# Kernel optimization log

Measured on AMD Instinct MI355X. Metric: run time of the kernel, lower is better.

Reference implementation:

```python
import jax, jax.numpy as jnp
import numpy as np

B, N, D, H, E = 4, 4096, 1024, 16, 256
HD = D // H  # head_dim = 64


def setup_inputs() -> dict:
    key = jax.random.key(0)
    k1, k2, k3, k4, k5 = jax.random.split(key, 5)
    scale = 1.0 / np.sqrt(D)
    return {
        "x": jax.random.normal(k1, (B, N, D), dtype=jnp.float32),
        "proj_weight_all": jax.random.normal(k2, (N, E), dtype=jnp.float32) * (1.0 / np.sqrt(N)),
        "W_q": jax.random.normal(k3, (D, D), dtype=jnp.float32) * scale,
        "W_k": jax.random.normal(k4, (D, D), dtype=jnp.float32) * scale,
        "W_v": jax.random.normal(k5, (D, D), dtype=jnp.float32) * scale,
    }


def reference(x, proj_weight_all, W_q, W_k, W_v):
    # QKV projections: [B,N,D] @ [D,D] -> [B,N,D]
    q = jnp.einsum('bnd,de->bne', x, W_q)
    k = jnp.einsum('bnd,de->bne', x, W_k)
    v = jnp.einsum('bnd,de->bne', x, W_v)
    # split heads -> [B,H,N,hd]
    split = lambda t: t.reshape(B, N, H, HD).transpose(0, 2, 1, 3)
    qh, kh, vh = split(q), split(k), split(v)
    # low-rank sequence projection of K/V: [B,H,N,hd] x [N,E] -> [B,H,E,hd]
    k_proj = jnp.einsum('bhnd,ne->bhed', kh, proj_weight_all)
    v_proj = jnp.einsum('bhnd,ne->bhed', vh, proj_weight_all)
    # attention over projected length E (dropout p=0 -> identity)
    scores = jnp.einsum('bhnd,bhed->bhne', qh, k_proj) / jnp.sqrt(jnp.float32(HD))
    attn = jax.nn.softmax(scores, axis=-1)  # [B,H,N,E]
    out = jnp.einsum('bhne,bhed->bhnd', attn, v_proj)
    # concat heads -> [B,N,D]
    return out.transpose(0, 2, 1, 3).reshape(B, N, D)
```

## Files before the change

### kernel.cpp

```cpp
#include <hip/hip_runtime.h>
#include <hip/hip_bf16.h>

#define B_ 4
#define N_ 4096
#define D_ 1024
#define H_ 16
#define E_ 256
#define HD_ 64

typedef __attribute__((ext_vector_type(8))) short bf16x8;
typedef __attribute__((ext_vector_type(4))) short shortx4;
typedef __attribute__((ext_vector_type(4))) float floatx4;

__device__ inline short f2bf(float f) {
  __hip_bfloat16 h = __float2bfloat16(f);
  short s;
  __builtin_memcpy(&s, &h, 2);
  return s;
}

__device__ inline void gld_lds16(const short* g, short* l) {
  __builtin_amdgcn_global_load_lds(
      (const __attribute__((address_space(1))) void*)g,
      (__attribute__((address_space(3))) void*)l, 16, 0, 0);
}

template <bool CAST_COPY>
__device__ inline void transpose_body(const float* __restrict__ src,
                                      short* __restrict__ dstT,
                                      short* __restrict__ dstC,
                                      int R, int C) {
  __shared__ float tile[32][33];
  int c0 = blockIdx.x * 32;
  int r0 = blockIdx.y * 32;
  int tx = threadIdx.x;
  int ty = threadIdx.y;
#pragma unroll
  for (int i = 0; i < 4; ++i) {
    int r = ty * 4 + i;
    float v = src[(size_t)(r0 + r) * C + (c0 + tx)];
    tile[r][tx] = v;
    if constexpr (CAST_COPY)
      dstC[(size_t)(r0 + r) * C + (c0 + tx)] = f2bf(v);
  }
  __syncthreads();
#pragma unroll
  for (int i = 0; i < 4; ++i) {
    int c = ty * 4 + i;
    dstT[(size_t)(c0 + c) * R + (r0 + tx)] = f2bf(tile[tx][c]);
  }
}

__global__ void transpose_x_kernel(const float* __restrict__ x,
                                   short* __restrict__ xtb,
                                   short* __restrict__ xb) {
  int b = blockIdx.z;
  transpose_body<true>(x + (size_t)b * N_ * D_, xtb + (size_t)b * D_ * N_,
                       xb + (size_t)b * N_ * D_, N_, D_);
}

__global__ void transpose_w_kernel(const float* __restrict__ Wq,
                                   const float* __restrict__ Wk,
                                   const float* __restrict__ Wv,
                                   short* __restrict__ WqT,
                                   short* __restrict__ WkT,
                                   short* __restrict__ WvT) {
  int z = blockIdx.z;
  const float* src = (z == 0) ? Wq : (z == 1) ? Wk : Wv;
  short* dst = (z == 0) ? WqT : (z == 1) ? WkT : WvT;
  transpose_body<false>(src, dst, nullptr, D_, D_);
}

__global__ void transpose_p_kernel(const float* __restrict__ proj,
                                   short* __restrict__ projT) {
  transpose_body<false>(proj, projT, nullptr, N_, E_);
}

__global__ void cast_f32_bf16_kernel(const float* __restrict__ in,
                                     short* __restrict__ out) {
  int i = (blockIdx.x * 256 + threadIdx.x) * 4;
  const float4 v = *(const float4*)(in + i);
  shortx4 o;
  o[0] = f2bf(v.x); o[1] = f2bf(v.y); o[2] = f2bf(v.z); o[3] = f2bf(v.w);
  *(shortx4*)(out + i) = o;
}

__global__ __launch_bounds__(256) void gemm128_bt_kernel(
    const short* __restrict__ Ag, const short* __restrict__ Btg,
    short* __restrict__ Cg, int M, int Nc, int K,
    long sA, long sB, long sC) {
  __shared__ short lds_a[128 * 32];
  __shared__ short lds_b[128 * 32];
  int tid = threadIdx.x;
  int lane = tid & 63;
  int w = tid >> 6;
  int l16 = lane & 15;
  int quad = lane >> 4;
  int wm = w >> 1, wn = w & 1;
  int m0 = blockIdx.x * 128, n0 = blockIdx.y * 128;

  const short* A = Ag + (size_t)blockIdx.z * sA;
  const short* Bt = Btg + (size_t)blockIdx.z * sB;
  short* C = Cg + (size_t)blockIdx.z * sC;

  int srow = tid >> 2;
  int skcol = (tid & 3) * 8;
  const short* ag = A + (size_t)(m0 + srow) * K + skcol;
  const short* bg = Bt + (size_t)(n0 + srow) * K + skcol;
  short* la = lds_a + tid * 8;
  short* lb = lds_b + tid * 8;
  const size_t half = (size_t)64 * K;

  floatx4 acc[4][4];
#pragma unroll
  for (int i = 0; i < 4; ++i)
#pragma unroll
    for (int j = 0; j < 4; ++j) acc[i][j] = (floatx4){0.f, 0.f, 0.f, 0.f};

  for (int k = 0; k < K; k += 32) {
    gld_lds16(ag + k, la);
    gld_lds16(ag + half + k, la + 64 * 32);
    gld_lds16(bg + k, lb);
    gld_lds16(bg + half + k, lb + 64 * 32);
    __syncthreads();

    bf16x8 af[4], bf[4];
#pragma unroll
    for (int mt = 0; mt < 4; ++mt)
      af[mt] = *(const bf16x8*)(lds_a + (wm * 64 + mt * 16 + l16) * 32 + quad * 8);
#pragma unroll
    for (int nt = 0; nt < 4; ++nt)
      bf[nt] = *(const bf16x8*)(lds_b + (wn * 64 + nt * 16 + l16) * 32 + quad * 8);
#pragma unroll
    for (int mt = 0; mt < 4; ++mt)
#pragma unroll
      for (int nt = 0; nt < 4; ++nt)
        acc[mt][nt] = __builtin_amdgcn_mfma_f32_16x16x32_bf16(af[mt], bf[nt], acc[mt][nt], 0, 0, 0);
    __syncthreads();
  }

#pragma unroll
  for (int mt = 0; mt < 4; ++mt)
#pragma unroll
    for (int nt = 0; nt < 4; ++nt)
#pragma unroll
      for (int r = 0; r < 4; ++r) {
        size_t row = (size_t)(m0 + wm * 64 + mt * 16 + quad * 4 + r);
        size_t col = (size_t)(n0 + wn * 64 + nt * 16 + l16);
        C[row * Nc + col] = f2bf(acc[mt][nt][r]);
      }
}

__global__ __launch_bounds__(256) void gemm128_splitk_kernel(
    const short* __restrict__ Ag, const short* __restrict__ Btg,
    float* __restrict__ Cfg, int M, int Nc, int K, int KS,
    long sA, long sB, long sC) {
  __shared__ short lds_a[128 * 32];
  __shared__ short lds_b[128 * 32];
  int tid = threadIdx.x;
  int lane = tid & 63;
  int w = tid >> 6;
  int l16 = lane & 15;
  int quad = lane >> 4;
  int wm = w >> 1, wn = w & 1;
  int m0 = blockIdx.x * 128, n0 = blockIdx.y * 128;
  int bz = blockIdx.z / KS;
  int ks = blockIdx.z % KS;
  int kchunk = K / KS;
  int k0 = ks * kchunk;

  const short* A = Ag + (size_t)bz * sA;
  const short* Bt = Btg + (size_t)bz * sB;
  float* Cf = Cfg + (size_t)bz * sC;

  int srow = tid >> 2;
  int skcol = (tid & 3) * 8;
  const short* ag = A + (size_t)(m0 + srow) * K + skcol;
  const short* bg = Bt + (size_t)(n0 + srow) * K + skcol;
  short* la = lds_a + tid * 8;
  short* lb = lds_b + tid * 8;
  const size_t half = (size_t)64 * K;

  floatx4 acc[4][4];
#pragma unroll
  for (int i = 0; i < 4; ++i)
#pragma unroll
    for (int j = 0; j < 4; ++j) acc[i][j] = (floatx4){0.f, 0.f, 0.f, 0.f};

  for (int k = k0; k < k0 + kchunk; k += 32) {
    gld_lds16(ag + k, la);
    gld_lds16(ag + half + k, la + 64 * 32);
    gld_lds16(bg + k, lb);
    gld_lds16(bg + half + k, lb + 64 * 32);
    __syncthreads();

    bf16x8 af[4], bf[4];
#pragma unroll
    for (int mt = 0; mt < 4; ++mt)
      af[mt] = *(const bf16x8*)(lds_a + (wm * 64 + mt * 16 + l16) * 32 + quad * 8);
#pragma unroll
    for (int nt = 0; nt < 4; ++nt)
      bf[nt] = *(const bf16x8*)(lds_b + (wn * 64 + nt * 16 + l16) * 32 + quad * 8);
#pragma unroll
    for (int mt = 0; mt < 4; ++mt)
#pragma unroll
      for (int nt = 0; nt < 4; ++nt)
        acc[mt][nt] = __builtin_amdgcn_mfma_f32_16x16x32_bf16(af[mt], bf[nt], acc[mt][nt], 0, 0, 0);
    __syncthreads();
  }

#pragma unroll
  for (int mt = 0; mt < 4; ++mt)
#pragma unroll
    for (int nt = 0; nt < 4; ++nt)
#pragma unroll
      for (int r = 0; r < 4; ++r) {
        size_t row = (size_t)(m0 + wm * 64 + mt * 16 + quad * 4 + r);
        size_t col = (size_t)(n0 + wn * 64 + nt * 16 + l16);
        atomicAdd(&Cf[row * Nc + col], acc[mt][nt][r]);
      }
}

__global__ __launch_bounds__(256) void gemm_kv_kernel(
    const short* __restrict__ xp, const short* __restrict__ WkT,
    const short* __restrict__ WvT, short* __restrict__ kpb,
    short* __restrict__ vpT) {
  int tid = threadIdx.x;
  int w = tid >> 6;
  int lane = tid & 63;
  int l16 = lane & 15;
  int quad = lane >> 4;
  int m_base = blockIdx.x * 64 + (w >> 1) * 32;
  int n_base = blockIdx.y * 64 + (w & 1) * 32;
  int b = blockIdx.z;

  const short* Ab = xp + (size_t)b * E_ * D_;
  short* Ck = kpb + (size_t)b * E_ * D_;
  short* Cv = vpT + (size_t)b * D_ * E_;

  floatx4 acck[2][2], accv[2][2];
#pragma unroll
  for (int i = 0; i < 2; ++i)
#pragma unroll
    for (int j = 0; j < 2; ++j) {
      acck[i][j] = (floatx4){0.f, 0.f, 0.f, 0.f};
      accv[i][j] = (floatx4){0.f, 0.f, 0.f, 0.f};
    }

  for (int k = 0; k < D_; k += 32) {
    bf16x8 a[2], bk[2], bv[2];
#pragma unroll
    for (int mt = 0; mt < 2; ++mt)
      a[mt] = *(const bf16x8*)(Ab + (size_t)(m_base + mt * 16 + l16) * D_ + k + quad * 8);
#pragma unroll
    for (int nt = 0; nt < 2; ++nt) {
      size_t off = (size_t)(n_base + nt * 16 + l16) * D_ + k + quad * 8;
      bk[nt] = *(const bf16x8*)(WkT + off);
      bv[nt] = *(const bf16x8*)(WvT + off);
    }
#pragma unroll
    for (int mt = 0; mt < 2; ++mt)
#pragma unroll
      for (int nt = 0; nt < 2; ++nt) {
        acck[mt][nt] = __builtin_amdgcn_mfma_f32_16x16x32_bf16(a[mt], bk[nt], acck[mt][nt], 0, 0, 0);
        accv[mt][nt] = __builtin_amdgcn_mfma_f32_16x16x32_bf16(a[mt], bv[nt], accv[mt][nt], 0, 0, 0);
      }
  }

#pragma unroll
  for (int mt = 0; mt < 2; ++mt)
#pragma unroll
    for (int nt = 0; nt < 2; ++nt)
#pragma unroll
      for (int r = 0; r < 4; ++r) {
        size_t row = (size_t)(m_base + mt * 16 + quad * 4 + r);
        size_t col = (size_t)(n_base + nt * 16 + l16);
        Ck[row * D_ + col] = f2bf(acck[mt][nt][r]);
        Cv[col * E_ + row] = f2bf(accv[mt][nt][r]);
      }
}

__global__ __launch_bounds__(512) void attn_kernel(
    const short* __restrict__ q,
    const short* __restrict__ kp,
    const short* __restrict__ vpT,
    float* __restrict__ out) {
  __shared__ short lds_kp_p[17408];
  __shared__ short lds_vp[16384];

  int tid = threadIdx.x;
  int w = tid >> 6;
  int lane = tid & 63;
  int l16 = lane & 15;
  int quad = lane >> 4;
  int n0 = blockIdx.x * 128;
  int h = blockIdx.y;
  int b = blockIdx.z;

  {
    const short* kpg = kp + (size_t)b * E_ * D_ + h * 64;
    int r0 = tid >> 3;
    int sseg = (tid & 7) ^ (r0 & 7);
#pragma unroll
    for (int j = 0; j < 4; ++j)
      gld_lds16(kpg + (size_t)(r0 + j * 64) * D_ + sseg * 8,
                lds_kp_p + j * 4096 + tid * 8);
  }
  {
    const short* vpg = vpT + (size_t)b * D_ * E_ + (size_t)(h * 64) * E_;
    int s1 = tid & 31;
    int rb = tid >> 5;
    int sseg = (s1 & 24) | ((s1 & 7) ^ (rb & 7));
#pragma unroll
    for (int j = 0; j < 4; ++j)
      gld_lds16(vpg + (size_t)(rb + j * 16) * E_ + sseg * 8,
                lds_vp + j * 4096 + tid * 8);
  }

  const short* qbase = q + ((size_t)(b * N_ + n0 + w * 16 + l16)) * D_ + h * 64;
  bf16x8 qf0 = *(const bf16x8*)(qbase + quad * 8);
  bf16x8 qf1 = *(const bf16x8*)(qbase + 32 + quad * 8);

  __syncthreads();

  floatx4 s[16];
#pragma unroll
  for (int t = 0; t < 16; ++t) s[t] = (floatx4){0.f, 0.f, 0.f, 0.f};

  int sw = l16 & 7;
#pragma unroll
  for (int t = 0; t < 16; ++t) {
    int r = t * 16 + l16;
    const short* rowp = lds_kp_p + r * 64;
    bf16x8 a0 = *(const bf16x8*)(rowp + ((quad) ^ sw) * 8);
    bf16x8 a1 = *(const bf16x8*)(rowp + ((4 + quad) ^ sw) * 8);
    s[t] = __builtin_amdgcn_mfma_f32_16x16x32_bf16(a0, qf0, s[t], 0, 0, 0);
    s[t] = __builtin_amdgcn_mfma_f32_16x16x32_bf16(a1, qf1, s[t], 0, 0, 0);
  }

  float mx = -1e30f;
#pragma unroll
  for (int t = 0; t < 16; ++t)
#pragma unroll
    for (int r = 0; r < 4; ++r) {
      s[t][r] *= 0.125f;
      mx = fmaxf(mx, s[t][r]);
    }
  mx = fmaxf(mx, __shfl_xor(mx, 16, 64));
  mx = fmaxf(mx, __shfl_xor(mx, 32, 64));

  float lsum = 0.f;
#pragma unroll
  for (int t = 0; t < 16; ++t)
#pragma unroll
    for (int r = 0; r < 4; ++r) {
      s[t][r] = __expf(s[t][r] - mx);
      lsum += s[t][r];
    }
  lsum += __shfl_xor(lsum, 16, 64);
  lsum += __shfl_xor(lsum, 32, 64);

  __syncthreads();

  short* pbase = lds_kp_p + w * 2176;
  floatx4 o4[4];
#pragma unroll
  for (int t2 = 0; t2 < 4; ++t2) o4[t2] = (floatx4){0.f, 0.f, 0.f, 0.f};

#pragma unroll
  for (int hf = 0; hf < 2; ++hf) {
#pragma unroll
    for (int t = 0; t < 8; ++t)
#pragma unroll
      for (int r = 0; r < 4; ++r)
        pbase[l16 * 136 + t * 16 + quad * 4 + r] = f2bf(s[hf * 8 + t][r]);

#pragma unroll
    for (int es2 = 0; es2 < 4; ++es2) {
      bf16x8 pa = *(const bf16x8*)(pbase + l16 * 136 + es2 * 32 + quad * 8);
      int es = hf * 4 + es2;
#pragma unroll
      for (int t2 = 0; t2 < 4; ++t2) {
        int rr = t2 * 16 + l16;
        int seg = es * 4 + quad;
        int sg = (seg & 24) | ((seg & 7) ^ sw);
        bf16x8 vf = *(const bf16x8*)(lds_vp + rr * 256 + sg * 8);
        o4[t2] = __builtin_amdgcn_mfma_f32_16x16x32_bf16(pa, vf, o4[t2], 0, 0, 0);
      }
    }
  }

  float linv[4];
#pragma unroll
  for (int r = 0; r < 4; ++r)
    linv[r] = 1.0f / __shfl(lsum, (lane & 48) | (quad * 4 + r), 64);

#pragma unroll
  for (int r = 0; r < 4; ++r) {
    int n = n0 + w * 16 + quad * 4 + r;
#pragma unroll
    for (int t2 = 0; t2 < 4; ++t2)
      out[((size_t)(b * N_ + n)) * D_ + h * 64 + t2 * 16 + l16] = o4[t2][r] * linv[r];
  }
}

extern "C" void kernel_launch(void* const* d_in, const int* in_sizes, int n_in,
                              void* d_out, int out_size, void* d_ws, size_t ws_size,
                              hipStream_t stream) {
  const float* x    = (const float*)d_in[0];
  const float* proj = (const float*)d_in[1];
  const float* Wq   = (const float*)d_in[2];
  const float* Wk   = (const float*)d_in[3];
  const float* Wv   = (const float*)d_in[4];
  float* out = (float*)d_out;

  short* p = (short*)d_ws;
  short* xtb_qb = p; p += (size_t)B_ * D_ * N_;
  short* xb     = p; p += (size_t)B_ * N_ * D_;
  short* WqT    = p; p += (size_t)D_ * D_;
  short* WkT    = p; p += (size_t)D_ * D_;
  short* WvT    = p; p += (size_t)D_ * D_;
  short* projT  = p; p += (size_t)E_ * N_;
  short* xp     = p; p += (size_t)B_ * E_ * D_;
  short* kpb    = p; p += (size_t)B_ * E_ * D_;
  short* vpT    = p; p += (size_t)B_ * D_ * E_;
  float* xp_f32 = (float*)p;
  short* xtb = xtb_qb;
  short* qb  = xtb_qb;

  dim3 blkT(32, 8);
  transpose_x_kernel<<<dim3(D_ / 32, N_ / 32, B_), blkT, 0, stream>>>(x, xtb, xb);
  transpose_w_kernel<<<dim3(D_ / 32, D_ / 32, 3), blkT, 0, stream>>>(Wq, Wk, Wv, WqT, WkT, WvT);
  transpose_p_kernel<<<dim3(E_ / 32, N_ / 32, 1), blkT, 0, stream>>>(proj, projT);

  hipMemsetAsync(xp_f32, 0, (size_t)B_ * E_ * D_ * sizeof(float), stream);
  const int KS = 8;
  gemm128_splitk_kernel<<<dim3(E_ / 128, D_ / 128, B_ * KS), 256, 0, stream>>>(
      projT, xtb, xp_f32, E_, D_, N_, KS, 0, (long)D_ * N_, (long)E_ * D_);
  cast_f32_bf16_kernel<<<(B_ * E_ * D_) / 1024, 256, 0, stream>>>(xp_f32, xp);

  gemm128_bt_kernel<<<dim3((B_ * N_) / 128, D_ / 128, 1), 256, 0, stream>>>(
      xb, WqT, qb, B_ * N_, D_, D_, 0, 0, 0);

  gemm_kv_kernel<<<dim3(E_ / 64, D_ / 64, B_), 256, 0, stream>>>(
      xp, WkT, WvT, kpb, vpT);

  attn_kernel<<<dim3(N_ / 128, H_, B_), 512, 0, stream>>>(qb, kpb, vpT, out);
}
```

Measured before the change: 302.2 us.

## Replace Q-projection GEMM with 256x256 tile, pipelined, swizzled-LDS kernel

Replaces the 128x128 single-buffered Q GEMM with a 512-thread 256x256 tile kernel. It double-buffers 128 KB of LDS, XOR-swizzles the LDS layout and interleaves async global-to-LDS loads with MFMA phases using explicit waitcnt, barriers and setprio. It also remaps block IDs for better L2 locality. This aims to hide load latency, cut LDS bank conflicts and raise operand reuse, at the cost of one block per CU and fewer blocks overall (256).

Result: faster. 285.6 us (-5.5%).

```diff
diff --git a/kernel.cpp b/kernel.cpp
--- a/kernel.cpp
+++ b/kernel.cpp
@@ -85,70 +85,171 @@
   *(shortx4*)(out + i) = o;
 }
 
-__global__ __launch_bounds__(256) void gemm128_bt_kernel(
+__device__ inline bf16x8 frag256(const short* slab, int row, int q) {
+  int a = (row << 6) + (q << 4);
+  a ^= ((a >> 7) & 7) << 4;
+  return *(const bf16x8*)(slab + (a >> 1));
+}
+
+#define G_BAR() __builtin_amdgcn_s_barrier()
+#define G_LGK0() asm volatile("s_waitcnt lgkmcnt(0)" ::: "memory")
+#define G_VM6() asm volatile("s_waitcnt vmcnt(6)" ::: "memory")
+#define G_VM0() asm volatile("s_waitcnt vmcnt(0)" ::: "memory")
+#define G_PRIO1() __builtin_amdgcn_s_setprio(1)
+#define G_PRIO0() __builtin_amdgcn_s_setprio(0)
+
+__global__ __launch_bounds__(512) void gemm256_bt_kernel(
     const short* __restrict__ Ag, const short* __restrict__ Btg,
-    short* __restrict__ Cg, int M, int Nc, int K,
-    long sA, long sB, long sC) {
-  __shared__ short lds_a[128 * 32];
-  __shared__ short lds_b[128 * 32];
+    short* __restrict__ Cg, int M, int Nc, int K) {
+  __shared__ short lds[65536];
+#define SLAB(b, o, kk2) (lds + ((((((b) << 1) | (o)) << 1) | (kk2)) * 8192))
+
   int tid = threadIdx.x;
   int lane = tid & 63;
   int w = tid >> 6;
   int l16 = lane & 15;
   int quad = lane >> 4;
-  int wm = w >> 1, wn = w & 1;
-  int m0 = blockIdx.x * 128, n0 = blockIdx.y * 128;
-
-  const short* A = Ag + (size_t)blockIdx.z * sA;
-  const short* Bt = Btg + (size_t)blockIdx.z * sB;
-  short* C = Cg + (size_t)blockIdx.z * sC;
-
-  int srow = tid >> 2;
-  int skcol = (tid & 3) * 8;
-  const short* ag = A + (size_t)(m0 + srow) * K + skcol;
-  const short* bg = Bt + (size_t)(n0 + srow) * K + skcol;
-  short* la = lds_a + tid * 8;
-  short* lb = lds_b + tid * 8;
-  const size_t half = (size_t)64 * K;
-
-  floatx4 acc[4][4];
-#pragma unroll
-  for (int i = 0; i < 4; ++i)
+  int wm = w >> 2;
+  int wn = w & 3;
+
+  int nwg = gridDim.x;
+  int cpx = nwg >> 3;
+  int bid = blockIdx.x;
+  int swz = (bid & 7) * cpx + (bid >> 3);
+  int ntile_m = M >> 8;
+  int tm = swz % ntile_m;
+  int tn = swz / ntile_m;
+  int m0 = tm * 256, n0 = tn * 256;
+
+  const short* gA = Ag + (size_t)m0 * K;
+  const short* gB = Btg + (size_t)n0 * K;
+
+  int a0 = tid * 16;
+  int w0 = a0 ^ (((a0 >> 7) & 7) << 4);
+  int a1 = (tid + 512) * 16;
+  int w1 = a1 ^ (((a1 >> 7) & 7) << 4);
+  size_t so0 = (size_t)(w0 >> 6) * K + ((w0 & 63) >> 1);
+  size_t so1 = (size_t)(w1 >> 6) * K + ((w1 & 63) >> 1);
+
+#define STAGE(b, o, kk2, gsrc)                      \
+  do {                                              \
+    short* _sl = SLAB(b, o, kk2);                   \
+    gld_lds16((gsrc) + so0, _sl + tid * 8);         \
+    gld_lds16((gsrc) + so1, _sl + 4096 + tid * 8);  \
+  } while (0)
+
+  floatx4 acc[8][4];
+#pragma unroll
+  for (int i = 0; i < 8; ++i)
 #pragma unroll
     for (int j = 0; j < 4; ++j) acc[i][j] = (floatx4){0.f, 0.f, 0.f, 0.f};
 
-  for (int k = 0; k < K; k += 32) {
-    gld_lds16(ag + k, la);
-    gld_lds16(ag + half + k, la + 64 * 32);
-    gld_lds16(bg + k, lb);
-    gld_lds16(bg + half + k, lb + 64 * 32);
-    __syncthreads();
-
-    bf16x8 af[4], bf[4];
-#pragma unroll
-    for (int mt = 0; mt < 4; ++mt)
-      af[mt] = *(const bf16x8*)(lds_a + (wm * 64 + mt * 16 + l16) * 32 + quad * 8);
+  bf16x8 af[8], bfr0, bfr1;
+
+#define READ_A(bu, kk2)                                             \
+  do {                                                              \
+    const short* _sa = SLAB(bu, 0, kk2);                            \
+    _Pragma("unroll") for (int mt = 0; mt < 8; ++mt)                \
+        af[mt] = frag256(_sa, wm * 128 + mt * 16 + l16, quad);      \
+  } while (0)
+#define READ_B(bu, kk2, ntb)                                        \
+  do {                                                              \
+    const short* _sb = SLAB(bu, 1, kk2);                            \
+    bfr0 = frag256(_sb, wn * 64 + (ntb)*16 + l16, quad);            \
+    bfr1 = frag256(_sb, wn * 64 + (ntb)*16 + 16 + l16, quad);       \
+  } while (0)
+#define MFMA2(c0, c1)                                                          \
+  do {                                                                         \
+    _Pragma("unroll") for (int mt = 0; mt < 8; ++mt) {                         \
+      acc[mt][c0] =                                                            \
+          __builtin_amdgcn_mfma_f32_16x16x32_bf16(af[mt], bfr0, acc[mt][c0],   \
+                                                  0, 0, 0);                    \
+      acc[mt][c1] =                                                            \
+          __builtin_amdgcn_mfma_f32_16x16x32_bf16(af[mt], bfr1, acc[mt][c1],   \
+                                                  0, 0, 0);                    \
+    }                                                                          \
+  } while (0)
+
+  STAGE(0, 0, 0, gA);
+  STAGE(0, 1, 0, gB);
+  STAGE(0, 0, 1, gA + 32);
+  STAGE(0, 1, 1, gB + 32);
+  STAGE(1, 0, 0, gA + 64);
+  STAGE(1, 1, 0, gB + 64);
+  STAGE(1, 0, 1, gA + 96);
+  G_VM6();
+  G_BAR();
+
+  const int NI = K >> 7;
+#pragma unroll 1
+  for (int it = 0; it < NI - 1; ++it) {
+    int t0 = it * 2;
+    const short* gAt2 = gA + (t0 + 2) * 64;
+    const short* gBt2 = gB + (t0 + 2) * 64;
+    const short* gAt3 = gA + (t0 + 3) * 64;
+    const short* gBt3 = gB + (t0 + 3) * 64;
+    READ_A(0, 0); READ_B(0, 0, 0);
+    STAGE(1, 1, 1, gB + (t0 + 1) * 64 + 32);
+    G_BAR(); G_LGK0(); G_PRIO1(); MFMA2(0, 1); G_PRIO0(); G_BAR();
+    READ_B(0, 0, 2);
+    STAGE(0, 0, 0, gAt2);
+    G_BAR(); G_LGK0(); G_PRIO1(); MFMA2(2, 3); G_PRIO0(); G_BAR();
+    READ_A(0, 1); READ_B(0, 1, 0);
+    STAGE(0, 1, 0, gBt2);
+    G_BAR(); G_LGK0(); G_PRIO1(); MFMA2(0, 1); G_PRIO0(); G_BAR();
+    READ_B(0, 1, 2);
+    STAGE(0, 0, 1, gAt2 + 32);
+    G_BAR(); G_LGK0(); G_PRIO1(); MFMA2(2, 3); G_PRIO0(); G_VM6(); G_BAR();
+    READ_A(1, 0); READ_B(1, 0, 0);
+    STAGE(0, 1, 1, gBt2 + 32);
+    G_BAR(); G_LGK0(); G_PRIO1(); MFMA2(0, 1); G_PRIO0(); G_BAR();
+    READ_B(1, 0, 2);
+    STAGE(1, 0, 0, gAt3);
+    G_BAR(); G_LGK0(); G_PRIO1(); MFMA2(2, 3); G_PRIO0(); G_BAR();
+    READ_A(1, 1); READ_B(1, 1, 0);
+    STAGE(1, 1, 0, gBt3);
+    G_BAR(); G_LGK0(); G_PRIO1(); MFMA2(0, 1); G_PRIO0(); G_BAR();
+    READ_B(1, 1, 2);
+    STAGE(1, 0, 1, gAt3 + 32);
+    G_BAR(); G_LGK0(); G_PRIO1(); MFMA2(2, 3); G_PRIO0(); G_VM6(); G_BAR();
+  }
+
+  {
+    int t0 = (NI - 1) * 2;
+    READ_A(0, 0); READ_B(0, 0, 0);
+    STAGE(1, 1, 1, gB + (t0 + 1) * 64 + 32);
+    G_BAR(); G_LGK0(); G_PRIO1(); MFMA2(0, 1); G_PRIO0(); G_BAR();
+    READ_B(0, 0, 2);
+    G_BAR(); G_LGK0(); G_PRIO1(); MFMA2(2, 3); G_PRIO0(); G_BAR();
+    READ_A(0, 1); READ_B(0, 1, 0);
+    G_BAR(); G_LGK0(); G_PRIO1(); MFMA2(0, 1); G_PRIO0(); G_BAR();
+    READ_B(0, 1, 2);
+    G_BAR(); G_LGK0(); G_PRIO1(); MFMA2(2, 3); G_PRIO0(); G_VM0(); G_BAR();
+    READ_A(1, 0); READ_B(1, 0, 0);
+    G_BAR(); G_LGK0(); G_PRIO1(); MFMA2(0, 1); G_PRIO0(); G_BAR();
+    READ_B(1, 0, 2);
+    G_BAR(); G_LGK0(); G_PRIO1(); MFMA2(2, 3); G_PRIO0(); G_BAR();
+    READ_A(1, 1); READ_B(1, 1, 0);
+    G_BAR(); G_LGK0(); G_PRIO1(); MFMA2(0, 1); G_PRIO0(); G_BAR();
+    READ_B(1, 1, 2);
+    G_BAR(); G_LGK0(); G_PRIO1(); MFMA2(2, 3); G_PRIO0();
+  }
+
+#pragma unroll
+  for (int mt = 0; mt < 8; ++mt)
 #pragma unroll
     for (int nt = 0; nt < 4; ++nt)
-      bf[nt] = *(const bf16x8*)(lds_b + (wn * 64 + nt * 16 + l16) * 32 + quad * 8);
-#pragma unroll
-    for (int mt = 0; mt < 4; ++mt)
-#pragma unroll
-      for (int nt = 0; nt < 4; ++nt)
-        acc[mt][nt] = __builtin_amdgcn_mfma_f32_16x16x32_bf16(af[mt], bf[nt], acc[mt][nt], 0, 0, 0);
-    __syncthreads();
-  }
-
-#pragma unroll
-  for (int mt = 0; mt < 4; ++mt)
-#pragma unroll
-    for (int nt = 0; nt < 4; ++nt)
 #pragma unroll
       for (int r = 0; r < 4; ++r) {
-        size_t row = (size_t)(m0 + wm * 64 + mt * 16 + quad * 4 + r);
+        size_t row = (size_t)(m0 + wm * 128 + mt * 16 + quad * 4 + r);
         size_t col = (size_t)(n0 + wn * 64 + nt * 16 + l16);
-        C[row * Nc + col] = f2bf(acc[mt][nt][r]);
+        Cg[row * Nc + col] = f2bf(acc[mt][nt][r]);
       }
+#undef SLAB
+#undef STAGE
+#undef READ_A
+#undef READ_B
+#undef MFMA2
 }
 
 __global__ __launch_bounds__(256) void gemm128_splitk_kernel(
@@ -439,8 +540,8 @@
       projT, xtb, xp_f32, E_, D_, N_, KS, 0, (long)D_ * N_, (long)E_ * D_);
   cast_f32_bf16_kernel<<<(B_ * E_ * D_) / 1024, 256, 0, stream>>>(xp_f32, xp);
 
-  gemm128_bt_kernel<<<dim3((B_ * N_) / 128, D_ / 128, 1), 256, 0, stream>>>(
-      xb, WqT, qb, B_ * N_, D_, D_, 0, 0, 0);
+  gemm256_bt_kernel<<<dim3(((B_ * N_) / 256) * (D_ / 256)), 512, 0, stream>>>(
+      xb, WqT, qb, B_ * N_, D_, D_);
 
   gemm_kv_kernel<<<dim3(E_ / 64, D_ / 64, B_), 256, 0, stream>>>(
       xp, WkT, WvT, kpb, vpT);
```
